# Performance work log

Hardware: AMD Instinct MI355X
Metric: run time of the kernel (lower is better)

## Reference

```python
import jax, jax.numpy as jnp
import numpy as np

D_K = 64
SCALE = 1.0 / np.sqrt(D_K).astype(np.float32)


def setup_inputs() -> dict:
    key = jax.random.key(0)
    kq, kk, kv = jax.random.split(key, 3)
    B, S, D = 4, 2048, 512
    q = jax.random.normal(kq, (B, S, D), dtype=jnp.float32)
    k = jax.random.normal(kk, (B, S, D), dtype=jnp.float32)
    v = jax.random.normal(kv, (B, S, D), dtype=jnp.float32)
    return {"q": q, "k": k, "v": v}


def reference(q, k, v):
    # n_head == 1: the per-head strided slices are the full tensors.
    # Original computes BOTH 'new_k' (scaled q@k^T) and 'new_v' (unscaled q@k^T);
    # note: v is never used in the original forward math (faithful reproduction).
    qk = jnp.einsum('bsd,btd->bst', q, k)           # [B, S, S]
    scores = qk * SCALE                              # new_k
    attn = jax.nn.softmax(scores, axis=2)            # softmax over dim 2
    # dropout with p=0.1 is identity in eval / deterministic reference
    out = jnp.matmul(attn, qk)                       # attn @ new_v -> [B, S, S]
    return out
```

## Files before the change

### kernel.cpp

```cpp
#include <hip/hip_runtime.h>
#include <hip/hip_bf16.h>
#include <stdint.h>


#define SS 2048
#define DD 512
#define BATCH 4
#define NTB 8
#define NT2A 32

typedef __attribute__((ext_vector_type(8))) short short8;
typedef __attribute__((ext_vector_type(8))) _Float16 half8;
typedef __attribute__((ext_vector_type(4))) float floatx4;
typedef __attribute__((ext_vector_type(4))) float float4v;
typedef __attribute__((ext_vector_type(4))) unsigned int uintx4;

#define GLOBAL_AS const __attribute__((address_space(1)))
#define LDS_AS __attribute__((address_space(3)))

__device__ __forceinline__ uint32_t pk2h(float x, float y) {
    _Float16 hx = (_Float16)x, hy = (_Float16)y;
    union { _Float16 h; uint16_t u; } cx, cy;
    cx.h = hx; cy.h = hy;
    return (uint32_t)cx.u | ((uint32_t)cy.u << 16);
}
__device__ __forceinline__ float h2f(uint32_t ubits) {
    union { uint16_t u; _Float16 h; } c; c.u = (uint16_t)ubits; return (float)c.h;
}
__device__ __forceinline__ uint16_t f2h(float f) {
    union { _Float16 h; uint16_t u; } c; c.h = (_Float16)f; return c.u;
}

union PackU { uint32_t u[4]; short8 s8; };

__global__ __launch_bounds__(256) void prep_kernel(
    const float* __restrict__ Q, const float* __restrict__ K,
    uint16_t* __restrict__ qT, uint16_t* __restrict__ qH,
    uint16_t* __restrict__ kH)
{
    const int b   = blockIdx.z;
    const int tid = threadIdx.x;

    if (blockIdx.y == 8) {
        const float* src = K + (size_t)b * SS * DD;
        uint16_t* dst = kH + (size_t)b * SS * DD;
        const int g0 = blockIdx.x * 256 + tid;
#pragma unroll
        for (int i = 0; i < 16; ++i) {
            const int g = g0 + i * 8192;
            const float4v* s4 = (const float4v*)(src + (size_t)g * 8);
            float4v x0 = s4[0], x1 = s4[1];
            PackU p;
            p.u[0] = pk2h(x0[0], x0[1]);
            p.u[1] = pk2h(x0[2], x0[3]);
            p.u[2] = pk2h(x1[0], x1[1]);
            p.u[3] = pk2h(x1[2], x1[3]);
            *(short8*)(dst + (size_t)g * 8) = p.s8;
        }
        return;
    }

    const int u0 = blockIdx.x * 64;
    const int d0 = blockIdx.y * 64;
    const float* qb = Q + (size_t)b * SS * DD;
    uint16_t* qTb = qT + (size_t)b * DD * SS;
    uint16_t* qHb = qH + (size_t)b * SS * DD;

    __shared__ uint16_t T[64 * 66];

    {
        const int r  = tid >> 2;
        const int c4 = (tid & 3) * 16;
        const float* src = qb + (size_t)(u0 + r) * DD + d0 + c4;
        float4v x0 = *(const float4v*)(src + 0);
        float4v x1 = *(const float4v*)(src + 4);
        float4v x2 = *(const float4v*)(src + 8);
        float4v x3 = *(const float4v*)(src + 12);
        uint32_t w0 = pk2h(x0[0], x0[1]), w1 = pk2h(x0[2], x0[3]);
        uint32_t w2 = pk2h(x1[0], x1[1]), w3 = pk2h(x1[2], x1[3]);
        uint32_t w4 = pk2h(x2[0], x2[1]), w5 = pk2h(x2[2], x2[3]);
        uint32_t w6 = pk2h(x3[0], x3[1]), w7 = pk2h(x3[2], x3[3]);
        uint32_t* tw = (uint32_t*)&T[r * 66 + c4];
        tw[0] = w0; tw[1] = w1; tw[2] = w2; tw[3] = w3;
        tw[4] = w4; tw[5] = w5; tw[6] = w6; tw[7] = w7;
        PackU p;
        p.u[0] = w0; p.u[1] = w1; p.u[2] = w2; p.u[3] = w3;
        *(short8*)(&qHb[(size_t)(u0 + r) * DD + d0 + c4]) = p.s8;
        p.u[0] = w4; p.u[1] = w5; p.u[2] = w6; p.u[3] = w7;
        *(short8*)(&qHb[(size_t)(u0 + r) * DD + d0 + c4 + 8]) = p.s8;
    }
    __syncthreads();
#pragma unroll
    for (int p = 0; p < 2; ++p) {
        const int dl  = (tid >> 3) + p * 32;
        const int ul8 = (tid & 7) * 8;
        uint16_t t8[8];
#pragma unroll
        for (int j = 0; j < 8; ++j) t8[j] = T[(ul8 + j) * 66 + dl];
        PackU o;
        o.u[0] = (uint32_t)t8[0] | ((uint32_t)t8[1] << 16);
        o.u[1] = (uint32_t)t8[2] | ((uint32_t)t8[3] << 16);
        o.u[2] = (uint32_t)t8[4] | ((uint32_t)t8[5] << 16);
        o.u[3] = (uint32_t)t8[6] | ((uint32_t)t8[7] << 16);
        *(short8*)(&qTb[(size_t)(d0 + dl) * SS + u0 + ul8]) = o.s8;
    }
}

__global__ __launch_bounds__(512, 2) void gemm1_kernel(
    const uint16_t* __restrict__ qH, const uint16_t* __restrict__ kH,
    uint16_t* __restrict__ qk)
{
    const int b  = blockIdx.z;
    const int s0 = blockIdx.y * 256;
    const int t0 = blockIdx.x * 256;
    const uint16_t* ab = qH + (size_t)b * SS * DD;
    const uint16_t* bb = kH + (size_t)b * SS * DD;

    __shared__ uint16_t smem[65536];

    const int tid  = threadIdx.x;
    const int lane = tid & 63;
    const int wave = tid >> 6;
    const int wm   = wave >> 2;
    const int wn   = wave & 3;
    const int fm   = lane & 15;
    const int quad = lane >> 4;

    floatx4 acc[8][4];
#pragma unroll
    for (int i = 0; i < 8; ++i)
#pragma unroll
        for (int j = 0; j < 4; ++j)
            acc[i][j] = (floatx4)0.0f;

    const int sl0  = (quad ^ (fm & 7)) * 8;
    const int aoff = (wm * 128 + fm) * 64;
    const int boff = 32768 + (wn * 64 + fm) * 64;

    const int c0 = wave * 128 + lane;
    const int r0 = c0 >> 3;  const int l0 = ((c0 & 7) ^ (r0 & 7)) * 8;
    const int c1 = c0 + 64;
    const int r1 = c1 >> 3;  const int l1 = ((c1 & 7) ^ (r1 & 7)) * 8;
    const int ldsW = wave * 1024;

    auto STAGE_A = [&](int tt, int h) {
        uint16_t* base = &smem[(tt & 1) * 16384 + h * 8192 + ldsW];
        __builtin_amdgcn_global_load_lds(
            (GLOBAL_AS void*)(ab + (size_t)(s0 + h * 128 + r0) * DD + tt * 64 + l0),
            (LDS_AS void*)(base), 16, 0, 0);
        __builtin_amdgcn_global_load_lds(
            (GLOBAL_AS void*)(ab + (size_t)(s0 + h * 128 + r1) * DD + tt * 64 + l1),
            (LDS_AS void*)(base + 512), 16, 0, 0);
    };
    auto STAGE_B = [&](int tt, int h) {
        uint16_t* base = &smem[32768 + (tt & 1) * 16384 + h * 8192 + ldsW];
        __builtin_amdgcn_global_load_lds(
            (GLOBAL_AS void*)(bb + (size_t)(t0 + h * 128 + r0) * DD + tt * 64 + l0),
            (LDS_AS void*)(base), 16, 0, 0);
        __builtin_amdgcn_global_load_lds(
            (GLOBAL_AS void*)(bb + (size_t)(t0 + h * 128 + r1) * DD + tt * 64 + l1),
            (LDS_AS void*)(base + 512), 16, 0, 0);
    };

    STAGE_A(0, 0); STAGE_A(0, 1); STAGE_B(0, 0); STAGE_B(0, 1);
    STAGE_B(1, 0); STAGE_B(1, 1);
    asm volatile("s_waitcnt vmcnt(4)" ::: "memory");
    __builtin_amdgcn_s_barrier();

    half8 aF[4], aF2[4], bF[4][2];

    for (int t = 0; t < NTB; ++t) {
        const int abase = (t & 1) * 16384;
        const int bbase = (t & 1) * 16384;

#pragma unroll
        for (int nt = 0; nt < 4; ++nt) {
            bF[nt][0] = *(const half8*)&smem[bbase + boff + nt * 1024 + sl0];
            bF[nt][1] = *(const half8*)&smem[bbase + boff + nt * 1024 + (sl0 ^ 32)];
        }
#pragma unroll
        for (int m = 0; m < 4; ++m)
            aF[m] = *(const half8*)&smem[abase + aoff + m * 1024 + sl0];
        if (t + 1 < NTB) STAGE_A(t + 1, 0);
        __builtin_amdgcn_s_barrier();
        asm volatile("s_waitcnt lgkmcnt(0)" ::: "memory");
        __builtin_amdgcn_s_setprio(1);
#pragma unroll
        for (int m = 0; m < 4; ++m)
#pragma unroll
            for (int nt = 0; nt < 4; ++nt)
                acc[m][nt] = __builtin_amdgcn_mfma_f32_16x16x32_f16(aF[m], bF[nt][0], acc[m][nt], 0, 0, 0);
        __builtin_amdgcn_s_setprio(0);
        __builtin_amdgcn_s_barrier();

#pragma unroll
        for (int m = 0; m < 4; ++m)
            aF2[m] = *(const half8*)&smem[abase + aoff + (m + 4) * 1024 + sl0];
        if (t + 1 < NTB) STAGE_A(t + 1, 1);
        __builtin_amdgcn_s_barrier();
        asm volatile("s_waitcnt lgkmcnt(0)" ::: "memory");
        __builtin_amdgcn_s_setprio(1);
#pragma unroll
        for (int m = 0; m < 4; ++m)
#pragma unroll
            for (int nt = 0; nt < 4; ++nt)
                acc[m + 4][nt] = __builtin_amdgcn_mfma_f32_16x16x32_f16(aF2[m], bF[nt][0], acc[m + 4][nt], 0, 0, 0);
        __builtin_amdgcn_s_setprio(0);
        __builtin_amdgcn_s_barrier();

#pragma unroll
        for (int m = 0; m < 4; ++m)
            aF[m] = *(const half8*)&smem[abase + aoff + m * 1024 + (sl0 ^ 32)];
        if (t + 2 < NTB) STAGE_B(t + 2, 0);
        __builtin_amdgcn_s_barrier();
        asm volatile("s_waitcnt lgkmcnt(0)" ::: "memory");
        __builtin_amdgcn_s_setprio(1);
#pragma unroll
        for (int m = 0; m < 4; ++m)
#pragma unroll
            for (int nt = 0; nt < 4; ++nt)
                acc[m][nt] = __builtin_amdgcn_mfma_f32_16x16x32_f16(aF[m], bF[nt][1], acc[m][nt], 0, 0, 0);
        __builtin_amdgcn_s_setprio(0);
        __builtin_amdgcn_s_barrier();

#pragma unroll
        for (int m = 0; m < 4; ++m)
            aF2[m] = *(const half8*)&smem[abase + aoff + (m + 4) * 1024 + (sl0 ^ 32)];
        if (t + 2 < NTB) {
            STAGE_B(t + 2, 1);
            asm volatile("s_waitcnt vmcnt(4)" ::: "memory");
        } else {
            asm volatile("s_waitcnt vmcnt(0)" ::: "memory");
        }
        __builtin_amdgcn_s_barrier();
        asm volatile("s_waitcnt lgkmcnt(0)" ::: "memory");
        __builtin_amdgcn_s_setprio(1);
#pragma unroll
        for (int m = 0; m < 4; ++m)
#pragma unroll
            for (int nt = 0; nt < 4; ++nt)
                acc[m + 4][nt] = __builtin_amdgcn_mfma_f32_16x16x32_f16(aF2[m], bF[nt][1], acc[m + 4][nt], 0, 0, 0);
        __builtin_amdgcn_s_setprio(0);
        __builtin_amdgcn_s_barrier();
    }

    uint16_t* ob = qk + (size_t)b * SS * SS;
#pragma unroll
    for (int mt = 0; mt < 8; ++mt) {
#pragma unroll
        for (int nt = 0; nt < 4; ++nt) {
            const int srow = s0 + wm * 128 + mt * 16 + quad * 4;
            const int tcol = t0 + wn * 64 + nt * 16 + fm;
#pragma unroll
            for (int reg = 0; reg < 4; ++reg)
                ob[(size_t)(srow + reg) * SS + tcol] = f2h(acc[mt][nt][reg]);
        }
    }
}

__global__ __launch_bounds__(256) void rowstats_kernel(
    const uint16_t* __restrict__ qk, float2* __restrict__ stats)
{
    const size_t row = blockIdx.x;
    const uint16_t* x = qk + row * SS;
    const int tid  = threadIdx.x;
    const int lane = tid & 63;
    const int wave = tid >> 6;

    uintx4 raw = *(const uintx4*)(x + tid * 8);
    float v[8];
#pragma unroll
    for (int i = 0; i < 4; ++i) {
        uint32_t u = raw[i];
        v[2 * i]     = h2f(u & 0xffffu) * 0.125f;
        v[2 * i + 1] = h2f(u >> 16) * 0.125f;
    }
    float m = v[0];
#pragma unroll
    for (int j = 1; j < 8; ++j) m = fmaxf(m, v[j]);
#pragma unroll
    for (int off = 1; off < 64; off <<= 1) m = fmaxf(m, __shfl_xor(m, off, 64));
    __shared__ float red[8];
    if (lane == 0) red[wave] = m;
    __syncthreads();
    m = fmaxf(fmaxf(red[0], red[1]), fmaxf(red[2], red[3]));

    float s = 0.f;
#pragma unroll
    for (int j = 0; j < 8; ++j) s += __expf(v[j] - m);
#pragma unroll
    for (int off = 1; off < 64; off <<= 1) s += __shfl_xor(s, off, 64);
    if (lane == 0) red[4 + wave] = s;
    __syncthreads();
    s = (red[4] + red[5]) + (red[6] + red[7]);
    if (tid == 0) stats[row] = make_float2(m, 1.0f / s);
}

__global__ __launch_bounds__(512, 2) void gemm2a_kernel(
    const uint16_t* __restrict__ qk, const uint16_t* __restrict__ qT,
    const float2* __restrict__ stats, uint16_t* __restrict__ tmp)
{
    const int b  = blockIdx.z;
    const int s0 = blockIdx.y * 128;
    const int t0 = blockIdx.x * 128;
    const uint16_t* ab = qk + (size_t)b * SS * SS;
    const uint16_t* bb = qT + (size_t)b * DD * SS;

    __shared__ uint16_t smem[32768];

    const int tid  = threadIdx.x;
    const int lane = tid & 63;
    const int wave = tid >> 6;
    const int wm   = wave >> 2;
    const int wn   = wave & 3;
    const int fm   = lane & 15;
    const int quad = lane >> 4;

    floatx4 acc[4][2];
#pragma unroll
    for (int i = 0; i < 4; ++i)
#pragma unroll
        for (int j = 0; j < 2; ++j)
            acc[i][j] = (floatx4)0.0f;

    const int sl0  = (quad ^ (fm & 7)) * 8;
    const int aoff = (wm * 64 + fm) * 64;
    const int boff = 16384 + (wn * 32 + fm) * 64;

    const int r0 = tid >> 3;
    const int l0 = (((tid & 7) ^ (r0 & 7))) * 8;
    const int r1 = r0 + 64;
    const int l1 = l0;
    const int ldsW = wave * 512;

    const float2 st0 = stats[(size_t)b * SS + s0 + r0];
    const float2 st1 = stats[(size_t)b * SS + s0 + r1];

    auto LOAD_A = [&](int tt, uintx4& ua, uintx4& ub) {
        ua = *(const uintx4*)(ab + (size_t)(s0 + r0) * SS + tt * 64 + l0);
        ub = *(const uintx4*)(ab + (size_t)(s0 + r1) * SS + tt * 64 + l1);
    };
    auto WRITE_A = [&](int tt, const uintx4& ua, const uintx4& ub) {
        uint16_t* base = &smem[(tt & 1) * 8192 + ldsW + lane * 8];
        PackU p;
#pragma unroll
        for (int j = 0; j < 4; ++j) {
            uint32_t u = ua[j];
            float va = h2f(u & 0xffffu) * 0.125f;
            float vb = h2f(u >> 16) * 0.125f;
            p.u[j] = pk2h(__expf(va - st0.x) * st0.y, __expf(vb - st0.x) * st0.y);
        }
        *(short8*)base = p.s8;
#pragma unroll
        for (int j = 0; j < 4; ++j) {
            uint32_t u = ub[j];
            float va = h2f(u & 0xffffu) * 0.125f;
            float vb = h2f(u >> 16) * 0.125f;
            p.u[j] = pk2h(__expf(va - st1.x) * st1.y, __expf(vb - st1.x) * st1.y);
        }
        *(short8*)(base + 4096) = p.s8;
    };
    auto STAGE_B = [&](int tt) {
        uint16_t* base = &smem[16384 + (tt & 1) * 8192 + ldsW];
        __builtin_amdgcn_global_load_lds(
            (GLOBAL_AS void*)(bb + (size_t)(t0 + r0) * SS + tt * 64 + l0),
            (LDS_AS void*)(base), 16, 0, 0);
        __builtin_amdgcn_global_load_lds(
            (GLOBAL_AS void*)(bb + (size_t)(t0 + r1) * SS + tt * 64 + l1),
            (LDS_AS void*)(base + 4096), 16, 0, 0);
    };

    uintx4 a0a, a0b, a1a, a1b;
    LOAD_A(0, a0a, a0b);
    LOAD_A(1, a1a, a1b);
    asm volatile("" ::: "memory");
    STAGE_B(0); STAGE_B(1);
    asm volatile("s_waitcnt vmcnt(2)" ::: "memory");
    WRITE_A(0, a0a, a0b);
    WRITE_A(1, a1a, a1b);
    asm volatile("s_waitcnt lgkmcnt(0)" ::: "memory");
    __builtin_amdgcn_s_barrier();

    half8 aF[4][2], bF[2][2];

    for (int t = 0; t < NT2A; ++t) {
        const int buf = (t & 1) * 8192;

        uintx4 nA0, nA1;
#pragma unroll
        for (int m = 0; m < 4; ++m) {
            aF[m][0] = *(const half8*)&smem[buf + aoff + m * 1024 + sl0];
            aF[m][1] = *(const half8*)&smem[buf + aoff + m * 1024 + (sl0 ^ 32)];
        }
#pragma unroll
        for (int n = 0; n < 2; ++n) {
            bF[n][0] = *(const half8*)&smem[buf + boff + n * 1024 + sl0];
            bF[n][1] = *(const half8*)&smem[buf + boff + n * 1024 + (sl0 ^ 32)];
        }
        if (t + 2 < NT2A) LOAD_A(t + 2, nA0, nA1);
        asm volatile("s_waitcnt lgkmcnt(0)" ::: "memory");
        __builtin_amdgcn_s_setprio(1);
#pragma unroll
        for (int m = 0; m < 4; ++m)
#pragma unroll
            for (int n = 0; n < 2; ++n)
                acc[m][n] = __builtin_amdgcn_mfma_f32_16x16x32_f16(aF[m][0], bF[n][0], acc[m][n], 0, 0, 0);
        __builtin_amdgcn_s_setprio(0);
        __builtin_amdgcn_s_barrier();

        if (t + 2 < NT2A) {
            STAGE_B(t + 2);
            asm volatile("s_waitcnt vmcnt(2)" ::: "memory");
            WRITE_A(t + 2, nA0, nA1);
            asm volatile("s_waitcnt lgkmcnt(0)" ::: "memory");
        } else {
            asm volatile("s_waitcnt vmcnt(0)" ::: "memory");
        }
        __builtin_amdgcn_s_barrier();
        __builtin_amdgcn_s_setprio(1);
#pragma unroll
        for (int m = 0; m < 4; ++m)
#pragma unroll
            for (int n = 0; n < 2; ++n)
                acc[m][n] = __builtin_amdgcn_mfma_f32_16x16x32_f16(aF[m][1], bF[n][1], acc[m][n], 0, 0, 0);
        __builtin_amdgcn_s_setprio(0);
    }

    uint16_t* tb = tmp + (size_t)b * SS * DD;
#pragma unroll
    for (int mt = 0; mt < 4; ++mt) {
#pragma unroll
        for (int n = 0; n < 2; ++n) {
            const int srw  = s0 + wm * 64 + mt * 16 + quad * 4;
            const int tcol = t0 + wn * 32 + n * 16 + fm;
#pragma unroll
            for (int reg = 0; reg < 4; ++reg)
                tb[(size_t)(srw + reg) * DD + tcol] = f2h(acc[mt][n][reg]);
        }
    }
}

__global__ __launch_bounds__(512, 2) void gemm2b_kernel(
    const uint16_t* __restrict__ tmp, const uint16_t* __restrict__ kH,
    float* __restrict__ out)
{
    const int b  = blockIdx.z;
    const int s0 = blockIdx.y * 256;
    const int t0 = blockIdx.x * 256;
    const uint16_t* ab = tmp + (size_t)b * SS * DD;
    const uint16_t* bb = kH  + (size_t)b * SS * DD;

    __shared__ uint16_t smem[65536];

    const int tid  = threadIdx.x;
    const int lane = tid & 63;
    const int wave = tid >> 6;
    const int wm   = wave >> 2;
    const int wn   = wave & 3;
    const int fm   = lane & 15;
    const int quad = lane >> 4;

    floatx4 acc[8][4];
#pragma unroll
    for (int i = 0; i < 8; ++i)
#pragma unroll
        for (int j = 0; j < 4; ++j)
            acc[i][j] = (floatx4)0.0f;

    const int sl0  = (quad ^ (fm & 7)) * 8;
    const int aoff = (wm * 128 + fm) * 64;
    const int boff = 32768 + (wn * 64 + fm) * 64;

    const int c0 = wave * 128 + lane;
    const int r0 = c0 >> 3;  const int l0 = ((c0 & 7) ^ (r0 & 7)) * 8;
    const int c1 = c0 + 64;
    const int r1 = c1 >> 3;  const int l1 = ((c1 & 7) ^ (r1 & 7)) * 8;
    const int ldsW = wave * 1024;

    auto STAGE_A = [&](int tt, int h) {
        uint16_t* base = &smem[(tt & 1) * 16384 + h * 8192 + ldsW];
        __builtin_amdgcn_global_load_lds(
            (GLOBAL_AS void*)(ab + (size_t)(s0 + h * 128 + r0) * DD + tt * 64 + l0),
            (LDS_AS void*)(base), 16, 0, 0);
        __builtin_amdgcn_global_load_lds(
            (GLOBAL_AS void*)(ab + (size_t)(s0 + h * 128 + r1) * DD + tt * 64 + l1),
            (LDS_AS void*)(base + 512), 16, 0, 0);
    };
    auto STAGE_B = [&](int tt, int h) {
        uint16_t* base = &smem[32768 + (tt & 1) * 16384 + h * 8192 + ldsW];
        __builtin_amdgcn_global_load_lds(
            (GLOBAL_AS void*)(bb + (size_t)(t0 + h * 128 + r0) * DD + tt * 64 + l0),
            (LDS_AS void*)(base), 16, 0, 0);
        __builtin_amdgcn_global_load_lds(
            (GLOBAL_AS void*)(bb + (size_t)(t0 + h * 128 + r1) * DD + tt * 64 + l1),
            (LDS_AS void*)(base + 512), 16, 0, 0);
    };

    STAGE_A(0, 0); STAGE_A(0, 1); STAGE_B(0, 0); STAGE_B(0, 1);
    STAGE_B(1, 0); STAGE_B(1, 1);
    asm volatile("s_waitcnt vmcnt(4)" ::: "memory");
    __builtin_amdgcn_s_barrier();

    half8 aF[4], aF2[4], bF[4][2];

    for (int t = 0; t < NTB; ++t) {
        const int abase = (t & 1) * 16384;
        const int bbase = (t & 1) * 16384;

#pragma unroll
        for (int nt = 0; nt < 4; ++nt) {
            bF[nt][0] = *(const half8*)&smem[bbase + boff + nt * 1024 + sl0];
            bF[nt][1] = *(const half8*)&smem[bbase + boff + nt * 1024 + (sl0 ^ 32)];
        }
#pragma unroll
        for (int m = 0; m < 4; ++m)
            aF[m] = *(const half8*)&smem[abase + aoff + m * 1024 + sl0];
        if (t + 1 < NTB) STAGE_A(t + 1, 0);
        __builtin_amdgcn_s_barrier();
        asm volatile("s_waitcnt lgkmcnt(0)" ::: "memory");
        __builtin_amdgcn_s_setprio(1);
#pragma unroll
        for (int m = 0; m < 4; ++m)
#pragma unroll
            for (int nt = 0; nt < 4; ++nt)
                acc[m][nt] = __builtin_amdgcn_mfma_f32_16x16x32_f16(aF[m], bF[nt][0], acc[m][nt], 0, 0, 0);
        __builtin_amdgcn_s_setprio(0);
        __builtin_amdgcn_s_barrier();

#pragma unroll
        for (int m = 0; m < 4; ++m)
            aF2[m] = *(const half8*)&smem[abase + aoff + (m + 4) * 1024 + sl0];
        if (t + 1 < NTB) STAGE_A(t + 1, 1);
        __builtin_amdgcn_s_barrier();
        asm volatile("s_waitcnt lgkmcnt(0)" ::: "memory");
        __builtin_amdgcn_s_setprio(1);
#pragma unroll
        for (int m = 0; m < 4; ++m)
#pragma unroll
            for (int nt = 0; nt < 4; ++nt)
                acc[m + 4][nt] = __builtin_amdgcn_mfma_f32_16x16x32_f16(aF2[m], bF[nt][0], acc[m + 4][nt], 0, 0, 0);
        __builtin_amdgcn_s_setprio(0);
        __builtin_amdgcn_s_barrier();

#pragma unroll
        for (int m = 0; m < 4; ++m)
            aF[m] = *(const half8*)&smem[abase + aoff + m * 1024 + (sl0 ^ 32)];
        if (t + 2 < NTB) STAGE_B(t + 2, 0);
        __builtin_amdgcn_s_barrier();
        asm volatile("s_waitcnt lgkmcnt(0)" ::: "memory");
        __builtin_amdgcn_s_setprio(1);
#pragma unroll
        for (int m = 0; m < 4; ++m)
#pragma unroll
            for (int nt = 0; nt < 4; ++nt)
                acc[m][nt] = __builtin_amdgcn_mfma_f32_16x16x32_f16(aF[m], bF[nt][1], acc[m][nt], 0, 0, 0);
        __builtin_amdgcn_s_setprio(0);
        __builtin_amdgcn_s_barrier();

#pragma unroll
        for (int m = 0; m < 4; ++m)
            aF2[m] = *(const half8*)&smem[abase + aoff + (m + 4) * 1024 + (sl0 ^ 32)];
        if (t + 2 < NTB) {
            STAGE_B(t + 2, 1);
            asm volatile("s_waitcnt vmcnt(4)" ::: "memory");
        } else {
            asm volatile("s_waitcnt vmcnt(0)" ::: "memory");
        }
        __builtin_amdgcn_s_barrier();
        asm volatile("s_waitcnt lgkmcnt(0)" ::: "memory");
        __builtin_amdgcn_s_setprio(1);
#pragma unroll
        for (int m = 0; m < 4; ++m)
#pragma unroll
            for (int nt = 0; nt < 4; ++nt)
                acc[m + 4][nt] = __builtin_amdgcn_mfma_f32_16x16x32_f16(aF2[m], bF[nt][1], acc[m + 4][nt], 0, 0, 0);
        __builtin_amdgcn_s_setprio(0);
        __builtin_amdgcn_s_barrier();
    }

    float* ob = out + (size_t)b * SS * SS;
#pragma unroll
    for (int mt = 0; mt < 8; ++mt) {
#pragma unroll
        for (int nt = 0; nt < 4; ++nt) {
            const int srow = s0 + wm * 128 + mt * 16 + quad * 4;
            const int tcol = t0 + wn * 64 + nt * 16 + fm;
#pragma unroll
            for (int reg = 0; reg < 4; ++reg)
                ob[(size_t)(srow + reg) * SS + tcol] = acc[mt][nt][reg];
        }
    }
}

extern "C" void kernel_launch(void* const* d_in, const int* in_sizes, int n_in,
                              void* d_out, int out_size, void* d_ws, size_t ws_size,
                              hipStream_t stream) {
    const float* q = (const float*)d_in[0];
    const float* k = (const float*)d_in[1];
    float* out = (float*)d_out;

    uint16_t* qk  = (uint16_t*)d_ws;
    uint16_t* qT  = qk + (size_t)BATCH * SS * SS;
    uint16_t* qH  = qT + (size_t)BATCH * DD * SS;
    uint16_t* kH  = qH + (size_t)BATCH * SS * DD;
    uint16_t* tmp = kH + (size_t)BATCH * SS * DD;
    float2* stats = (float2*)(tmp + (size_t)BATCH * SS * DD);

    prep_kernel<<<dim3(32, 9, BATCH), 256, 0, stream>>>(q, k, qT, qH, kH);
    gemm1_kernel<<<dim3(SS / 256, SS / 256, BATCH), 512, 0, stream>>>(qH, kH, qk);
    rowstats_kernel<<<dim3(BATCH * SS), 256, 0, stream>>>(qk, stats);
    gemm2a_kernel<<<dim3(DD / 128, SS / 128, BATCH), 512, 0, stream>>>(qk, qT, stats, tmp);
    gemm2b_kernel<<<dim3(SS / 256, SS / 256, BATCH), 512, 0, stream>>>(tmp, kH, out);
}
```

Measured before the change: 204.4 us.

## Triple-buffer A tile in gemm2a to hide global load latency

Moves the A operand (the softmax-transformed qk tile) in gemm2a to a three-slot LDS ring and issues its global load three iterations ahead. The exp/scale/write into LDS now happens before the first MFMA half instead of after the mid-iteration barrier. The aim is to hide global load latency and move the transform work off the barrier-critical path. In exchange LDS use per block grows from 64KB to 80KB, which could limit the two-blocks-per-CU occupancy, and more registers are needed to hold the in-flight loads.

```diff
diff --git a/kernel.cpp b/kernel.cpp
--- a/kernel.cpp
+++ b/kernel.cpp
@@ -306,7 +306,7 @@
     const uint16_t* ab = qk + (size_t)b * SS * SS;
     const uint16_t* bb = qT + (size_t)b * DD * SS;
 
-    __shared__ uint16_t smem[32768];
+    __shared__ uint16_t smem[40960];
 
     const int tid  = threadIdx.x;
     const int lane = tid & 63;
@@ -325,12 +325,11 @@
 
     const int sl0  = (quad ^ (fm & 7)) * 8;
     const int aoff = (wm * 64 + fm) * 64;
-    const int boff = 16384 + (wn * 32 + fm) * 64;
+    const int boff = 24576 + (wn * 32 + fm) * 64;
 
     const int r0 = tid >> 3;
-    const int l0 = (((tid & 7) ^ (r0 & 7))) * 8;
+    const int l0 = ((tid & 7) ^ (r0 & 7)) * 8;
     const int r1 = r0 + 64;
-    const int l1 = l0;
     const int ldsW = wave * 512;
 
     const float2 st0 = stats[(size_t)b * SS + s0 + r0];
@@ -338,10 +337,10 @@
 
     auto LOAD_A = [&](int tt, uintx4& ua, uintx4& ub) {
         ua = *(const uintx4*)(ab + (size_t)(s0 + r0) * SS + tt * 64 + l0);
-        ub = *(const uintx4*)(ab + (size_t)(s0 + r1) * SS + tt * 64 + l1);
+        ub = *(const uintx4*)(ab + (size_t)(s0 + r1) * SS + tt * 64 + l0);
     };
-    auto WRITE_A = [&](int tt, const uintx4& ua, const uintx4& ub) {
-        uint16_t* base = &smem[(tt & 1) * 8192 + ldsW + lane * 8];
+    auto WRITE_A = [&](int wbuf, const uintx4& ua, const uintx4& ub) {
+        uint16_t* base = &smem[wbuf * 8192 + ldsW + lane * 8];
         PackU p;
 #pragma unroll
         for (int j = 0; j < 4; ++j) {
@@ -361,43 +360,47 @@
         *(short8*)(base + 4096) = p.s8;
     };
     auto STAGE_B = [&](int tt) {
-        uint16_t* base = &smem[16384 + (tt & 1) * 8192 + ldsW];
+        uint16_t* base = &smem[24576 + (tt & 1) * 8192 + ldsW];
         __builtin_amdgcn_global_load_lds(
             (GLOBAL_AS void*)(bb + (size_t)(t0 + r0) * SS + tt * 64 + l0),
             (LDS_AS void*)(base), 16, 0, 0);
         __builtin_amdgcn_global_load_lds(
-            (GLOBAL_AS void*)(bb + (size_t)(t0 + r1) * SS + tt * 64 + l1),
+            (GLOBAL_AS void*)(bb + (size_t)(t0 + r1) * SS + tt * 64 + l0),
             (LDS_AS void*)(base + 4096), 16, 0, 0);
     };
 
-    uintx4 a0a, a0b, a1a, a1b;
-    LOAD_A(0, a0a, a0b);
-    LOAD_A(1, a1a, a1b);
+    uintx4 w0a, w0b, w1a, w1b, cur0, cur1;
+    uintx4 nxt0 = {}, nxt1 = {};
+    LOAD_A(0, w0a, w0b);
+    LOAD_A(1, w1a, w1b);
+    LOAD_A(2, cur0, cur1);
     asm volatile("" ::: "memory");
     STAGE_B(0); STAGE_B(1);
-    asm volatile("s_waitcnt vmcnt(2)" ::: "memory");
-    WRITE_A(0, a0a, a0b);
-    WRITE_A(1, a1a, a1b);
+    WRITE_A(0, w0a, w0b);
+    WRITE_A(1, w1a, w1b);
+    asm volatile("s_waitcnt vmcnt(0)" ::: "memory");
     asm volatile("s_waitcnt lgkmcnt(0)" ::: "memory");
     __builtin_amdgcn_s_barrier();
 
     half8 aF[4][2], bF[2][2];
+    int rdA = 0, wrA = 2;
 
     for (int t = 0; t < NT2A; ++t) {
-        const int buf = (t & 1) * 8192;
-
-        uintx4 nA0, nA1;
+        const int abase = rdA * 8192;
+        const int bbase = (t & 1) * 8192;
+
 #pragma unroll
         for (int m = 0; m < 4; ++m) {
-            aF[m][0] = *(const half8*)&smem[buf + aoff + m * 1024 + sl0];
-            aF[m][1] = *(const half8*)&smem[buf + aoff + m * 1024 + (sl0 ^ 32)];
+            aF[m][0] = *(const half8*)&smem[abase + aoff + m * 1024 + sl0];
+            aF[m][1] = *(const half8*)&smem[abase + aoff + m * 1024 + (sl0 ^ 32)];
         }
 #pragma unroll
         for (int n = 0; n < 2; ++n) {
-            bF[n][0] = *(const half8*)&smem[buf + boff + n * 1024 + sl0];
-            bF[n][1] = *(const half8*)&smem[buf + boff + n * 1024 + (sl0 ^ 32)];
-        }
-        if (t + 2 < NT2A) LOAD_A(t + 2, nA0, nA1);
+            bF[n][0] = *(const half8*)&smem[bbase + boff + n * 1024 + sl0];
+            bF[n][1] = *(const half8*)&smem[bbase + boff + n * 1024 + (sl0 ^ 32)];
+        }
+        if (t + 3 < NT2A) LOAD_A(t + 3, nxt0, nxt1);
+        if (t + 2 < NT2A) WRITE_A(wrA, cur0, cur1);
         asm volatile("s_waitcnt lgkmcnt(0)" ::: "memory");
         __builtin_amdgcn_s_setprio(1);
 #pragma unroll
@@ -410,9 +413,11 @@
 
         if (t + 2 < NT2A) {
             STAGE_B(t + 2);
-            asm volatile("s_waitcnt vmcnt(2)" ::: "memory");
-            WRITE_A(t + 2, nA0, nA1);
-            asm volatile("s_waitcnt lgkmcnt(0)" ::: "memory");
+            if (t + 3 < NT2A) {
+                asm volatile("s_waitcnt vmcnt(4)" ::: "memory");
+            } else {
+                asm volatile("s_waitcnt vmcnt(2)" ::: "memory");
+            }
         } else {
             asm volatile("s_waitcnt vmcnt(0)" ::: "memory");
         }
@@ -424,6 +429,10 @@
             for (int n = 0; n < 2; ++n)
                 acc[m][n] = __builtin_amdgcn_mfma_f32_16x16x32_f16(aF[m][1], bF[n][1], acc[m][n], 0, 0, 0);
         __builtin_amdgcn_s_setprio(0);
+
+        cur0 = nxt0; cur1 = nxt1;
+        rdA = (rdA == 2) ? 0 : rdA + 1;
+        wrA = (wrA == 2) ? 0 : wrA + 1;
     }
 
     uint16_t* tb = tmp + (size_t)b * SS * DD;
```

Measured after the change: 199.0 us. 2.6% less time.
